# Optimization experiments

Measured on AMD Instinct MI355X. Metric: run time of the kernel, lower is better.

## Reference

```python
import jax, jax.numpy as jnp
import numpy as np

B, NPTS = 4, 16384          # clouds, points per cloud (equal-size batches)
DX, DP = 3, 3               # feature dim, coordinate dim -> pos6d is 6-D
RATIO, R, MAX_NB = 0.25, 0.25, 64


def setup_inputs() -> dict:
    key = jax.random.key(0)
    k1, k2 = jax.random.split(key)
    x = jax.random.uniform(k1, (B * NPTS, DX), dtype=jnp.float32)
    pos = jax.random.uniform(k2, (B * NPTS, DP), dtype=jnp.float32)
    # contiguous equal-size batch ids (sorted), as torch_geometric expects
    batch = jnp.repeat(jnp.arange(B, dtype=jnp.int32), NPTS)
    return {"x": x, "pos": pos, "batch": batch}


def _fps(p, m):
    """Farthest point sampling on [n, d] points; returns m int32 indices.
    Deterministic start at index 0 (torch_cluster uses a random start)."""
    n = p.shape[0]

    def step(carry, _):
        mind, last = carry
        d = jnp.sum((p - p[last]) ** 2, axis=-1)       # dist^2 to last pick
        mind = jnp.minimum(mind, d)
        nxt = jnp.argmax(mind).astype(jnp.int32)
        return (mind, nxt), last

    init = (jnp.full((n,), jnp.inf, p.dtype), jnp.int32(0))
    _, idx = jax.lax.scan(step, init, None, length=m)
    return idx                                         # [m]


def reference(x, pos, batch):
    dx = x.shape[1]
    m = int(RATIO * NPTS)                              # centers per cloud
    pos6 = jnp.concatenate([x, pos], axis=-1).reshape(B, NPTS, -1)  # [B,n,6]
    xb = x.reshape(B, NPTS, dx)

    # FPS in 6-D, per cloud
    idx_local = jax.vmap(lambda p: _fps(p, m))(pos6)   # [B, m]
    centers = jnp.take_along_axis(pos6, idx_local[:, :, None], axis=1)  # [B,m,6]

    r2 = R * R
    arange_n = jnp.arange(NPTS, dtype=jnp.int32)
    outs = []
    for b in range(B):  # small fixed loop keeps the [m,n] dist matrix per-cloud
        d2 = jnp.sum((centers[b][:, None, :] - pos6[b][None, :, :]) ** 2, axis=-1)  # [m,n]
        # radius neighbors, capped at MAX_NB, first-in-index-order (torch_cluster-like)
        key_idx = jnp.where(d2 <= r2, arange_n, NPTS)
        neg, cols = jax.lax.top_k(-key_idx, MAX_NB)    # smallest valid indices
        w = (-neg < NPTS).astype(x.dtype)              # [m, MAX_NB] validity
        feats = xb[b][cols]                            # [m, MAX_NB, dx]
        # scatter_mean over row ids == masked mean per center (self always valid)
        outs.append(jnp.einsum('mk,mkd->md', w, feats) / jnp.sum(w, axis=1, keepdims=True))

    x_centers = jnp.concatenate(outs, axis=0)          # [B*m, dx]
    idx_g = (idx_local + (jnp.arange(B, dtype=jnp.int32) * NPTS)[:, None]).reshape(-1)
    return x_centers, pos[idx_g], batch[idx_g]
```

## Files before the change

kernel.cpp:

```cpp
#include <hip/hip_runtime.h>
#include <math.h>

#define BATCH 4
#define NPTS 16384
#define M 4096
#define MAX_NB 64
#define R2F 0.0625f
#define FPS_T 512
#define PPT 32

__device__ __forceinline__ float dist2_fma(
    float a0, float a1, float a2, float a3, float a4, float a5,
    float b0, float b1, float b2, float b3, float b4, float b5) {
  float d0 = a0 - b0;
  float s = __builtin_fmaf(d0, d0, 0.0f);
  float d1 = a1 - b1; s = __builtin_fmaf(d1, d1, s);
  float d2 = a2 - b2; s = __builtin_fmaf(d2, d2, s);
  float d3 = a3 - b3; s = __builtin_fmaf(d3, d3, s);
  float d4 = a4 - b4; s = __builtin_fmaf(d4, d4, s);
  float d5 = a5 - b5; s = __builtin_fmaf(d5, d5, s);
  return s;
}

__device__ __forceinline__ float dist2_seq(
    float a0, float a1, float a2, float a3, float a4, float a5,
    float b0, float b1, float b2, float b3, float b4, float b5) {
#pragma clang fp contract(off)
  float d0 = a0 - b0; float s = d0 * d0;
  float d1 = a1 - b1; s = s + d1 * d1;
  float d2 = a2 - b2; s = s + d2 * d2;
  float d3 = a3 - b3; s = s + d3 * d3;
  float d4 = a4 - b4; s = s + d4 * d4;
  float d5 = a5 - b5; s = s + d5 * d5;
  return s;
}

__global__
__attribute__((amdgpu_flat_work_group_size(FPS_T, FPS_T)))
__attribute__((amdgpu_waves_per_eu(2, 2)))
void fps_kernel(
    const float* __restrict__ x, const float* __restrict__ pos,
    float* __restrict__ out) {
  __shared__ float s_rv[FPS_T / 64];
  __shared__ int s_ri[FPS_T / 64];
  __shared__ int s_g;

  const int b = blockIdx.x;
  const int t = threadIdx.x;
  const float* xb = x + (size_t)b * NPTS * 3;
  const float* pb = pos + (size_t)b * NPTS * 3;

  float* out_pos = out + (size_t)BATCH * M * 3;
  int* idx_stash = (int*)(out + (size_t)2 * BATCH * M * 3);

  float c0[PPT], c1[PPT], c2[PPT], c3[PPT], c4[PPT], c5[PPT], mind[PPT];
#pragma unroll
  for (int j = 0; j < PPT; ++j) {
    const int p = j * FPS_T + t;
    c0[j] = xb[3 * p + 0];
    c1[j] = xb[3 * p + 1];
    c2[j] = xb[3 * p + 2];
    c3[j] = pb[3 * p + 0];
    c4[j] = pb[3 * p + 1];
    c5[j] = pb[3 * p + 2];
    mind[j] = INFINITY;
  }

  int g = 0;
  for (int k = 0; k < M; ++k) {
    const float fx0 = xb[3 * g + 0];
    const float fx1 = xb[3 * g + 1];
    const float fx2 = xb[3 * g + 2];
    const float fx3 = pb[3 * g + 0];
    const float fx4 = pb[3 * g + 1];
    const float fx5 = pb[3 * g + 2];

    if (t == 0) {
      idx_stash[b * M + k] = g;
      out_pos[(size_t)(b * M + k) * 3 + 0] = fx3;
      out_pos[(size_t)(b * M + k) * 3 + 1] = fx4;
      out_pos[(size_t)(b * M + k) * 3 + 2] = fx5;
    }
    if (k == M - 1) break;

    float bestv = -1.0f;
    int bestj = 0;
#pragma unroll
    for (int j = 0; j < PPT; ++j) {
      const float d2 = dist2_fma(c0[j], c1[j], c2[j], c3[j], c4[j], c5[j],
                                 fx0, fx1, fx2, fx3, fx4, fx5);
      const float nm = fminf(mind[j], d2);
      mind[j] = nm;
      if (nm > bestv) {
        bestv = nm;
        bestj = j;
      }
    }
    int besti = bestj * FPS_T + t;

#pragma unroll
    for (int off = 32; off > 0; off >>= 1) {
      const float ov = __shfl_xor(bestv, off, 64);
      const int oi = __shfl_xor(besti, off, 64);
      if (ov > bestv || (ov == bestv && oi < besti)) {
        bestv = ov;
        besti = oi;
      }
    }
    const int w = t >> 6;
    if ((t & 63) == 0) {
      s_rv[w] = bestv;
      s_ri[w] = besti;
    }
    __syncthreads();
    if (t == 0) {
      float bv = s_rv[0];
      int bi = s_ri[0];
#pragma unroll
      for (int ww = 1; ww < FPS_T / 64; ++ww) {
        const float v = s_rv[ww];
        const int i2 = s_ri[ww];
        if (v > bv || (v == bv && i2 < bi)) {
          bv = v;
          bi = i2;
        }
      }
      s_g = bi;
    }
    __syncthreads();
    g = __builtin_amdgcn_readfirstlane(s_g);
  }
}

#define K2_T 256
__global__ __launch_bounds__(K2_T, 4) void nbr_kernel(
    const float* __restrict__ x, const float* __restrict__ pos,
    float* __restrict__ out) {
  const int lane = threadIdx.x & 63;
  const int w = threadIdx.x >> 6;
  const int cbase = blockIdx.x * 16 + w * 4;

  const int* idx_stash = (const int*)(out + (size_t)2 * BATCH * M * 3);
  float* out_x = out;
  float* out_batch = out + (size_t)2 * BATCH * M * 3;

  const int b = cbase / M;
  const float* xb = x + (size_t)b * NPTS * 3;
  const float* pb = pos + (size_t)b * NPTS * 3;

  float cc0[4], cc1[4], cc2[4], cc3[4], cc4[4], cc5[4];
#pragma unroll
  for (int i = 0; i < 4; ++i) {
    const int c = idx_stash[cbase + i];
    cc0[i] = xb[3 * c + 0];
    cc1[i] = xb[3 * c + 1];
    cc2[i] = xb[3 * c + 2];
    cc3[i] = pb[3 * c + 0];
    cc4[i] = pb[3 * c + 1];
    cc5[i] = pb[3 * c + 2];
  }

  float s0[4] = {0, 0, 0, 0}, s1[4] = {0, 0, 0, 0}, s2[4] = {0, 0, 0, 0};
  int cnt[4] = {0, 0, 0, 0};

  for (int p = lane; p < NPTS; p += 64) {
    const float x0 = xb[3 * p + 0];
    const float x1 = xb[3 * p + 1];
    const float x2 = xb[3 * p + 2];
    const float q0 = pb[3 * p + 0];
    const float q1 = pb[3 * p + 1];
    const float q2 = pb[3 * p + 2];
#pragma unroll
    for (int i = 0; i < 4; ++i) {
      const float d2 = dist2_seq(cc0[i], cc1[i], cc2[i], cc3[i], cc4[i],
                                 cc5[i], x0, x1, x2, q0, q1, q2);
      if (d2 <= R2F) {
        cnt[i] += 1;
        s0[i] += x0;
        s1[i] += x1;
        s2[i] += x2;
      }
    }
  }

#pragma unroll
  for (int i = 0; i < 4; ++i) {
#pragma unroll
    for (int off = 32; off > 0; off >>= 1) {
      s0[i] += __shfl_xor(s0[i], off, 64);
      s1[i] += __shfl_xor(s1[i], off, 64);
      s2[i] += __shfl_xor(s2[i], off, 64);
      cnt[i] += __shfl_xor(cnt[i], off, 64);
    }
  }

#pragma unroll
  for (int i = 0; i < 4; ++i) {
    const int total = cnt[i];
    float m0, m1, m2;
    if (total <= MAX_NB) {
      const float denom = (float)total;
      m0 = s0[i] / denom;
      m1 = s1[i] / denom;
      m2 = s2[i] / denom;
    } else {
      const int base = lane * (NPTS / 64);
      int lc = 0;
      for (int p = base; p < base + NPTS / 64; ++p) {
        const float d2 =
            dist2_seq(cc0[i], cc1[i], cc2[i], cc3[i], cc4[i], cc5[i],
                      xb[3 * p + 0], xb[3 * p + 1], xb[3 * p + 2],
                      pb[3 * p + 0], pb[3 * p + 1], pb[3 * p + 2]);
        if (d2 <= R2F) lc += 1;
      }
      int pre = 0;
      for (int l = 0; l < 64; ++l) {
        const int c = __shfl(lc, l, 64);
        if (l < lane) pre += c;
      }
      float t0 = 0, t1 = 0, t2 = 0;
      int r = pre;
      for (int p = base; p < base + NPTS / 64; ++p) {
        const float x0 = xb[3 * p + 0], x1 = xb[3 * p + 1],
                    x2 = xb[3 * p + 2];
        const float d2 =
            dist2_seq(cc0[i], cc1[i], cc2[i], cc3[i], cc4[i], cc5[i], x0, x1,
                      x2, pb[3 * p + 0], pb[3 * p + 1], pb[3 * p + 2]);
        if (d2 <= R2F) {
          if (r < MAX_NB) {
            t0 += x0;
            t1 += x1;
            t2 += x2;
          }
          r += 1;
        }
      }
#pragma unroll
      for (int off = 32; off > 0; off >>= 1) {
        t0 += __shfl_xor(t0, off, 64);
        t1 += __shfl_xor(t1, off, 64);
        t2 += __shfl_xor(t2, off, 64);
      }
      m0 = t0 / 64.0f;
      m1 = t1 / 64.0f;
      m2 = t2 / 64.0f;
    }
    if (lane == i) {
      const int gc = cbase + i;
      out_x[(size_t)gc * 3 + 0] = m0;
      out_x[(size_t)gc * 3 + 1] = m1;
      out_x[(size_t)gc * 3 + 2] = m2;
      out_batch[gc] = (float)b;
    }
  }
}

extern "C" void kernel_launch(void* const* d_in, const int* in_sizes, int n_in,
                              void* d_out, int out_size, void* d_ws,
                              size_t ws_size, hipStream_t stream) {
  (void)in_sizes;
  (void)n_in;
  (void)out_size;
  (void)d_ws;
  (void)ws_size;
  const float* x = (const float*)d_in[0];
  const float* pos = (const float*)d_in[1];
  float* out = (float*)d_out;

  fps_kernel<<<BATCH, FPS_T, 0, stream>>>(x, pos, out);
  nbr_kernel<<<(BATCH * M) / 16, K2_T, 0, stream>>>(x, pos, out);
}
```

Before: 9.444 ms.

## Split FPS per cloud across four blocks with atomic inter-block argmax exchange

Farthest point sampling for each cloud is now spread across 4 workgroups, so each thread holds 8 points instead of 32 and the per-iteration distance and min update work per block shrinks. Every iteration, each block publishes its best candidate as a packed 64-bit key (iteration, distance bits, inverted index) to a double-buffered global slot array. It then spin-waits on the other blocks' slots and reduces to a common next point. This trades serial per-block compute for a device-scope global memory round trip and spin synchronisation on every one of the ~4096 iterations. It also relies on all 16 blocks being co-resident and on a memset of the slot array before launch.

```diff
diff --git a/kernel.cpp b/kernel.cpp
--- a/kernel.cpp
+++ b/kernel.cpp
@@ -6,8 +6,11 @@
 #define M 4096
 #define MAX_NB 64
 #define R2F 0.0625f
+
+#define KS 4
 #define FPS_T 512
-#define PPT 32
+#define PPB (NPTS / KS)
+#define PPT (PPB / FPS_T)
 
 __device__ __forceinline__ float dist2_fma(
     float a0, float a1, float a2, float a3, float a4, float a5,
@@ -40,12 +43,13 @@
 __attribute__((amdgpu_waves_per_eu(2, 2)))
 void fps_kernel(
     const float* __restrict__ x, const float* __restrict__ pos,
-    float* __restrict__ out) {
+    float* __restrict__ out, unsigned long long* __restrict__ slots) {
   __shared__ float s_rv[FPS_T / 64];
   __shared__ int s_ri[FPS_T / 64];
   __shared__ int s_g;
 
-  const int b = blockIdx.x;
+  const int b = blockIdx.x & (KS - 1);
+  const int sblk = blockIdx.x >> 2;
   const int t = threadIdx.x;
   const float* xb = x + (size_t)b * NPTS * 3;
   const float* pb = pos + (size_t)b * NPTS * 3;
@@ -53,10 +57,12 @@
   float* out_pos = out + (size_t)BATCH * M * 3;
   int* idx_stash = (int*)(out + (size_t)2 * BATCH * M * 3);
 
+  const int pbase = sblk * PPB;
+
   float c0[PPT], c1[PPT], c2[PPT], c3[PPT], c4[PPT], c5[PPT], mind[PPT];
 #pragma unroll
   for (int j = 0; j < PPT; ++j) {
-    const int p = j * FPS_T + t;
+    const int p = pbase + j * FPS_T + t;
     c0[j] = xb[3 * p + 0];
     c1[j] = xb[3 * p + 1];
     c2[j] = xb[3 * p + 2];
@@ -75,7 +81,7 @@
     const float fx4 = pb[3 * g + 1];
     const float fx5 = pb[3 * g + 2];
 
-    if (t == 0) {
+    if (sblk == 0 && t == 0) {
       idx_stash[b * M + k] = g;
       out_pos[(size_t)(b * M + k) * 3 + 0] = fx3;
       out_pos[(size_t)(b * M + k) * 3 + 1] = fx4;
@@ -96,7 +102,7 @@
         bestj = j;
       }
     }
-    int besti = bestj * FPS_T + t;
+    int besti = pbase + bestj * FPS_T + t;
 
 #pragma unroll
     for (int off = 32; off > 0; off >>= 1) {
@@ -113,7 +119,8 @@
       s_ri[w] = besti;
     }
     __syncthreads();
-    if (t == 0) {
+
+    if (t < 64) {
       float bv = s_rv[0];
       int bi = s_ri[0];
 #pragma unroll
@@ -125,7 +132,29 @@
           bi = i2;
         }
       }
-      s_g = bi;
+      unsigned long long key =
+          ((unsigned long long)(unsigned)(k + 1) << 46) |
+          ((unsigned long long)__float_as_uint(bv) << 14) |
+          (unsigned long long)(unsigned)(16383 - bi);
+      unsigned long long* set =
+          slots + (size_t)(((k & 1) * BATCH + b) * KS);
+      if (t == 0) {
+        __hip_atomic_store(&set[sblk], key, __ATOMIC_RELAXED,
+                           __HIP_MEMORY_SCOPE_AGENT);
+      }
+      unsigned long long other = key;
+      if (t < KS && t != sblk) {
+        do {
+          other = __hip_atomic_load(&set[t], __ATOMIC_RELAXED,
+                                    __HIP_MEMORY_SCOPE_AGENT);
+        } while ((other >> 46) < (unsigned long long)(unsigned)(k + 1));
+      }
+#pragma unroll
+      for (int off = 1; off < KS; off <<= 1) {
+        const unsigned long long o = __shfl_xor(other, off, 64);
+        if (o > other) other = o;
+      }
+      if (t == 0) s_g = 16383 - (int)(other & 0x3FFFull);
     }
     __syncthreads();
     g = __builtin_amdgcn_readfirstlane(s_g);
@@ -261,12 +290,17 @@
   (void)in_sizes;
   (void)n_in;
   (void)out_size;
-  (void)d_ws;
-  (void)ws_size;
   const float* x = (const float*)d_in[0];
   const float* pos = (const float*)d_in[1];
   float* out = (float*)d_out;
 
-  fps_kernel<<<BATCH, FPS_T, 0, stream>>>(x, pos, out);
+  const size_t slot_bytes =
+      (size_t)2 * BATCH * KS * sizeof(unsigned long long);
+  unsigned long long* slots = (ws_size >= slot_bytes)
+                                  ? (unsigned long long*)d_ws
+                                  : (unsigned long long*)d_out;
+  hipMemsetAsync(slots, 0, slot_bytes, stream);
+
+  fps_kernel<<<BATCH * KS, FPS_T, 0, stream>>>(x, pos, out, slots);
   nbr_kernel<<<(BATCH * M) / 16, K2_T, 0, stream>>>(x, pos, out);
 }
```

Result: slower. 10.05 ms (+6.5%).

## Double FPS block size, move coords to LDS, use barrier-free packed-key argmax

Applied to the files above, without the earlier changes.

The FPS kernel now runs 1024 threads per cloud, so each thread holds 16 points instead of 32. Two of the six coordinate arrays move from registers into LDS to relieve register pressure. The two-barrier block argmax is replaced by a 64-bit packed key (distance bits plus inverted index) reduced with single shuffles. Each wave publishes its key to a double-buffered LDS slot tagged with the iteration number and spin-waits on the other waves' slots. This removes the per-iteration __syncthreads on the serial 4096-step loop. The cost is extra LDS reads per point and a spin-wait that depends on relaxed atomics and on waves making progress.

```diff
diff --git a/kernel.cpp b/kernel.cpp
--- a/kernel.cpp
+++ b/kernel.cpp
@@ -6,8 +6,10 @@
 #define M 4096
 #define MAX_NB 64
 #define R2F 0.0625f
-#define FPS_T 512
-#define PPT 32
+
+#define FPS_T 1024
+#define WPB (FPS_T / 64)
+#define PPT (NPTS / FPS_T)
 
 __device__ __forceinline__ float dist2_fma(
     float a0, float a1, float a2, float a3, float a4, float a5,
@@ -37,23 +39,28 @@
 
 __global__
 __attribute__((amdgpu_flat_work_group_size(FPS_T, FPS_T)))
-__attribute__((amdgpu_waves_per_eu(2, 2)))
+__attribute__((amdgpu_waves_per_eu(4, 4)))
 void fps_kernel(
     const float* __restrict__ x, const float* __restrict__ pos,
     float* __restrict__ out) {
-  __shared__ float s_rv[FPS_T / 64];
-  __shared__ int s_ri[FPS_T / 64];
-  __shared__ int s_g;
+  __shared__ float s_c4[NPTS];
+  __shared__ float s_c5[NPTS];
+  __shared__ unsigned long long s_wk[2][WPB];
 
   const int b = blockIdx.x;
   const int t = threadIdx.x;
+  const int w = t >> 6;
+  const int lane = t & 63;
+
   const float* xb = x + (size_t)b * NPTS * 3;
   const float* pb = pos + (size_t)b * NPTS * 3;
 
   float* out_pos = out + (size_t)BATCH * M * 3;
   int* idx_stash = (int*)(out + (size_t)2 * BATCH * M * 3);
 
-  float c0[PPT], c1[PPT], c2[PPT], c3[PPT], c4[PPT], c5[PPT], mind[PPT];
+  if (t < 2 * WPB) s_wk[t >> 4][t & (WPB - 1)] = 0ull;
+
+  float c0[PPT], c1[PPT], c2[PPT], c3[PPT], mind[PPT];
 #pragma unroll
   for (int j = 0; j < PPT; ++j) {
     const int p = j * FPS_T + t;
@@ -61,10 +68,11 @@
     c1[j] = xb[3 * p + 1];
     c2[j] = xb[3 * p + 2];
     c3[j] = pb[3 * p + 0];
-    c4[j] = pb[3 * p + 1];
-    c5[j] = pb[3 * p + 2];
+    s_c4[p] = pb[3 * p + 1];
+    s_c5[p] = pb[3 * p + 2];
     mind[j] = INFINITY;
   }
+  __syncthreads();
 
   int g = 0;
   for (int k = 0; k < M; ++k) {
@@ -87,7 +95,10 @@
     int bestj = 0;
 #pragma unroll
     for (int j = 0; j < PPT; ++j) {
-      const float d2 = dist2_fma(c0[j], c1[j], c2[j], c3[j], c4[j], c5[j],
+      const int p = j * FPS_T + t;
+      const float a4 = s_c4[p];
+      const float a5 = s_c5[p];
+      const float d2 = dist2_fma(c0[j], c1[j], c2[j], c3[j], a4, a5,
                                  fx0, fx1, fx2, fx3, fx4, fx5);
       const float nm = fminf(mind[j], d2);
       mind[j] = nm;
@@ -96,39 +107,37 @@
         bestj = j;
       }
     }
-    int besti = bestj * FPS_T + t;
-
+    const int besti = bestj * FPS_T + t;
+
+    unsigned long long kk =
+        ((unsigned long long)__float_as_uint(bestv) << 14) |
+        (unsigned long long)(unsigned)(16383 - besti);
 #pragma unroll
     for (int off = 32; off > 0; off >>= 1) {
-      const float ov = __shfl_xor(bestv, off, 64);
-      const int oi = __shfl_xor(besti, off, 64);
-      if (ov > bestv || (ov == bestv && oi < besti)) {
-        bestv = ov;
-        besti = oi;
-      }
-    }
-    const int w = t >> 6;
-    if ((t & 63) == 0) {
-      s_rv[w] = bestv;
-      s_ri[w] = besti;
-    }
-    __syncthreads();
-    if (t == 0) {
-      float bv = s_rv[0];
-      int bi = s_ri[0];
-#pragma unroll
-      for (int ww = 1; ww < FPS_T / 64; ++ww) {
-        const float v = s_rv[ww];
-        const int i2 = s_ri[ww];
-        if (v > bv || (v == bv && i2 < bi)) {
-          bv = v;
-          bi = i2;
-        }
-      }
-      s_g = bi;
-    }
-    __syncthreads();
-    g = __builtin_amdgcn_readfirstlane(s_g);
+      const unsigned long long o = __shfl_xor(kk, off, 64);
+      if (o > kk) kk = o;
+    }
+
+    const int par = k & 1;
+    const unsigned long long want = (unsigned long long)(unsigned)(k + 1);
+
+    if (lane == 0) {
+      __hip_atomic_store(&s_wk[par][w], (want << 46) | kk, __ATOMIC_RELAXED,
+                         __HIP_MEMORY_SCOPE_WORKGROUP);
+    }
+
+    unsigned long long got;
+    do {
+      got = __hip_atomic_load(&s_wk[par][lane & (WPB - 1)], __ATOMIC_RELAXED,
+                              __HIP_MEMORY_SCOPE_WORKGROUP);
+    } while ((got >> 46) < want);
+#pragma unroll
+    for (int off = 1; off < WPB; off <<= 1) {
+      const unsigned long long o = __shfl_xor(got, off, 64);
+      if (o > got) got = o;
+    }
+    g = __builtin_amdgcn_readfirstlane(
+        16383 - (int)(got & 0x3FFFull));
   }
 }
 
```

New measurement: 12.16 ms. 28.7% more time.
